# Kernel tuning notes

Measured on AMD Instinct MI355X. Metric: run time of the kernel, lower is better.

## Reference

```python
import jax, jax.numpy as jnp
import numpy as np

B, T, D, H, L = 512, 1024, 2, 32, 16  # batch, seq_len, input_dim, hidden_dim, latent_dim


def lstm_layer(x, W_ih, W_hh, b_ih, b_hh):
    """Single torch-semantics LSTM layer. x: [B, T, D_in] -> (h_seq [B,T,H], c_final [B,H]).
    Gate order matches torch: i, f, g, o."""
    Bb = x.shape[0]
    Hh = W_hh.shape[1]
    # Precompute input projection for all timesteps (one big GEMM).
    xW = jnp.einsum('btd,gd->btg', x, W_ih) + (b_ih + b_hh)  # [B, T, 4H]

    def step(carry, xw_t):
        h, c = carry
        gates = xw_t + h @ W_hh.T  # [B, 4H]
        i, f, g, o = jnp.split(gates, 4, axis=-1)
        i = jax.nn.sigmoid(i)
        f = jax.nn.sigmoid(f)
        g = jnp.tanh(g)
        o = jax.nn.sigmoid(o)
        c = f * c + i * g
        h = o * jnp.tanh(c)
        return (h, c), h

    h0 = jnp.zeros((Bb, Hh), x.dtype)
    c0 = jnp.zeros((Bb, Hh), x.dtype)
    (_, cT), h_seq = jax.lax.scan(step, (h0, c0), jnp.swapaxes(xW, 0, 1))
    return jnp.swapaxes(h_seq, 0, 1), cT


def setup_inputs() -> dict:
    key = jax.random.key(0)
    ks = jax.random.split(key, 20)
    s = 1.0 / np.sqrt(H)  # torch LSTM/Linear init scale
    u = lambda k, shape: jax.random.uniform(k, shape, jnp.float32, -s, s)
    inp = {"x": jax.random.normal(ks[0], (B, T, D), jnp.float32)}
    dims_in = [D, H, H]
    for l in range(3):
        inp[f"W_ih{l}"] = u(ks[1 + 4 * l], (4 * H, dims_in[l]))
        inp[f"W_hh{l}"] = u(ks[2 + 4 * l], (4 * H, H))
        inp[f"b_ih{l}"] = u(ks[3 + 4 * l], (4 * H,))
        inp[f"b_hh{l}"] = u(ks[4 + 4 * l], (4 * H,))
    inp["W_mean"] = u(ks[13], (L, H))
    inp["b_mean"] = u(ks[14], (L,))
    inp["W_logvar"] = u(ks[15], (L, H))
    inp["b_logvar"] = u(ks[16], (L,))
    return inp


def reference(x, W_ih0, W_hh0, b_ih0, b_hh0, W_ih1, W_hh1, b_ih1, b_hh1,
              W_ih2, W_hh2, b_ih2, b_hh2, W_mean, b_mean, W_logvar, b_logvar):
    # 3-layer LSTM (dropout inactive at inference); only top-layer final cell is used.
    h, _ = lstm_layer(x, W_ih0, W_hh0, b_ih0, b_hh0)
    h, _ = lstm_layer(h, W_ih1, W_hh1, b_ih1, b_hh1)
    _, c3 = lstm_layer(h, W_ih2, W_hh2, b_ih2, b_hh2)  # c3: [B, H]
    mean = c3 @ W_mean.T + b_mean        # [B, L]
    log_var = c3 @ W_logvar.T + b_logvar  # [B, L]
    return (mean, log_var)
```

## Files before the change

kernel.cpp:

```cpp
#include <hip/hip_runtime.h>

#define T_LEN 1024
#define HID   32
#define LDIM  16
#define BATCH 512
#define NT    384

typedef _Float16 h2 __attribute__((ext_vector_type(2)));
typedef unsigned int u32;

#if defined(__has_builtin)
#if __has_builtin(__builtin_amdgcn_fdot2)
#define HAVE_FDOT2 1
#endif
#if __has_builtin(__builtin_amdgcn_rcpf)
#define FAST_RCP(x) __builtin_amdgcn_rcpf(x)
#endif
#endif
#ifndef FAST_RCP
#define FAST_RCP(x) (1.0f / (x))
#endif

__device__ __forceinline__ float dot2acc(u32 w, u32 h, float acc) {
#ifdef HAVE_FDOT2
    return __builtin_amdgcn_fdot2(__builtin_bit_cast(h2, w),
                                  __builtin_bit_cast(h2, h), acc, false);
#else
    h2 a = __builtin_bit_cast(h2, w);
    h2 b = __builtin_bit_cast(h2, h);
    return acc + (float)a[0] * (float)b[0] + (float)a[1] * (float)b[1];
#endif
}

__device__ __forceinline__ u32 packh2(float a, float b) {
    h2 v;
    v[0] = (_Float16)a;
    v[1] = (_Float16)b;
    return __builtin_bit_cast(u32, v);
}

template <int OFF>
__device__ __forceinline__ float swz(float v) {
    return __builtin_bit_cast(float,
        __builtin_amdgcn_ds_swizzle(__builtin_bit_cast(int, v), OFF));
}

__global__ __launch_bounds__(NT, 3)
void lstm_encoder_kernel(const float* __restrict__ x,
                         const float* __restrict__ Wih0, const float* __restrict__ Whh0,
                         const float* __restrict__ bih0, const float* __restrict__ bhh0,
                         const float* __restrict__ Wih1, const float* __restrict__ Whh1,
                         const float* __restrict__ bih1, const float* __restrict__ bhh1,
                         const float* __restrict__ Wih2, const float* __restrict__ Whh2,
                         const float* __restrict__ bih2, const float* __restrict__ bhh2,
                         const float* __restrict__ Wm,  const float* __restrict__ bm,
                         const float* __restrict__ Wlv, const float* __restrict__ blv,
                         float* __restrict__ out)
{
    const int b    = blockIdx.x;
    const int tid  = threadIdx.x;
    const int lane = tid & 63;
    const int wave = tid >> 6;
    const int l    = wave >> 1;
    const int wv   = wave & 1;
    const int q    = (lane >> 3) & 3;
    const int e    = (lane & 7) | ((lane >> 2) & 8);
    const int j    = wv * 16 + e;
    const int r = ((q & 1) ? 64 : 0) + ((q & 2) ? 32 : 0) + j;

    __shared__ float xs[T_LEN * 2];
    __shared__ __align__(16) _Float16 hb0[3][HID];
    __shared__ __align__(16) _Float16 hb1[3][HID];
    __shared__ float cbuf[HID];

    const float4* xb4 = (const float4*)(x + (size_t)b * (T_LEN * 2));
    for (int i = tid; i < (T_LEN * 2) / 4; i += NT) ((float4*)xs)[i] = xb4[i];

    if (tid < 48)       ((u32*)hb0)[tid]      = 0u;
    else if (tid < 96)  ((u32*)hb1)[tid - 48] = 0u;

    const float* Wih = (l == 0) ? Wih0 : (l == 1) ? Wih1 : Wih2;
    const float* Whh = (l == 0) ? Whh0 : (l == 1) ? Whh1 : Whh2;
    const float* bih = (l == 0) ? bih0 : (l == 1) ? bih1 : bih2;
    const float* bhh = (l == 0) ? bhh0 : (l == 1) ? bhh1 : bhh2;

    u32 wpack[32];
    float wx0 = 0.f, wx1 = 0.f;
#pragma unroll
    for (int k = 0; k < 16; ++k)
        wpack[16 + k] = packh2(Whh[r * HID + 2 * k], Whh[r * HID + 2 * k + 1]);
    if (l == 0) {
        wx0 = Wih[r * 2 + 0];
        wx1 = Wih[r * 2 + 1];
#pragma unroll
        for (int k = 0; k < 16; ++k) wpack[k] = 0u;
    } else {
#pragma unroll
        for (int k = 0; k < 16; ++k)
            wpack[k] = packh2(Wih[r * HID + 2 * k], Wih[r * HID + 2 * k + 1]);
    }
    const float bias = bih[r] + bhh[r];
#pragma unroll
    for (int k = 0; k < 32; ++k) asm volatile("" : "+v"(wpack[k]));

    const bool  is_g = (q == 1);
    const float kneg = is_g ? -2.0f : -1.0f;
    const float mm   = is_g ?  2.0f :  1.0f;
    const float aa   = is_g ? -1.0f :  0.0f;

    float c = 0.0f;

    __syncthreads();

#define STEP(RD, WR, S)                                                          \
    do {                                                                         \
        const int t_ = (S) - l;                                                  \
        if ((unsigned)t_ < (unsigned)T_LEN) {                                    \
            float a0 = bias, a1 = 0.f, a2 = 0.f, a3 = 0.f;                       \
            if (l == 0) {                                                        \
                const float2 xv = *(const float2*)&xs[2 * t_];                   \
                a0 = fmaf(wx0, xv.x, a0);                                        \
                a1 = fmaf(wx1, xv.y, a1);                                        \
                const uint4* hv = (const uint4*)&RD[0][0];                       \
                _Pragma("unroll")                                                \
                for (int k = 0; k < 4; ++k) {                                    \
                    const uint4 h = hv[k];                                       \
                    a0 = dot2acc(wpack[16 + 4 * k + 0], h.x, a0);                \
                    a1 = dot2acc(wpack[16 + 4 * k + 1], h.y, a1);                \
                    a2 = dot2acc(wpack[16 + 4 * k + 2], h.z, a2);                \
                    a3 = dot2acc(wpack[16 + 4 * k + 3], h.w, a3);                \
                }                                                                \
            } else {                                                             \
                const uint4* hv = (const uint4*)&RD[l - 1][0];                   \
                _Pragma("unroll")                                                \
                for (int k = 0; k < 8; ++k) {                                    \
                    const uint4 h = hv[k];                                       \
                    a0 = dot2acc(wpack[4 * k + 0], h.x, a0);                     \
                    a1 = dot2acc(wpack[4 * k + 1], h.y, a1);                     \
                    a2 = dot2acc(wpack[4 * k + 2], h.z, a2);                     \
                    a3 = dot2acc(wpack[4 * k + 3], h.w, a3);                     \
                }                                                                \
            }                                                                    \
            const float pre = (a0 + a1) + (a2 + a3);                             \
            const float ex  = __expf(kneg * pre);                                \
            const float y   = fmaf(mm, FAST_RCP(1.0f + ex), aa);                 \
            const float y1  = swz<0x201F>(y);           \
            const float P   = y * y1;                   \
            const float v   = (q < 2) ? P : y;                                   \
            const float z   = swz<0x401F>(v);         \
            c = fmaf(y, c, z);                             \
            const float e2 = __expf(-2.0f * c);                                  \
            const float th = fmaf(2.0f, FAST_RCP(1.0f + e2), -1.0f);             \
            if (q == 2) WR[l][j] = (_Float16)(y1 * th);        \
        }                                                                        \
        __syncthreads();                                                         \
    } while (0)

    for (int s = 0; s < T_LEN + 2; s += 2) {
        STEP(hb0, hb1, s);
        STEP(hb1, hb0, s + 1);
    }
#undef STEP

    if (l == 2 && q == 2) cbuf[j] = c;
    __syncthreads();

    if (tid < 2 * LDIM) {
        const bool   is_mean = (tid < LDIM);
        const int    jo = is_mean ? tid : tid - LDIM;
        const float* W  = is_mean ? Wm  : Wlv;
        const float* Bb = is_mean ? bm  : blv;
        float acc = Bb[jo];
#pragma unroll
        for (int k = 0; k < HID; ++k) acc = fmaf(W[jo * HID + k], cbuf[k], acc);
        const size_t off = (is_mean ? 0 : (size_t)BATCH * LDIM) + (size_t)b * LDIM + jo;
        out[off] = acc;
    }
}

extern "C" void kernel_launch(void* const* d_in, const int* in_sizes, int n_in,
                              void* d_out, int out_size, void* d_ws, size_t ws_size,
                              hipStream_t stream) {
    const float* x    = (const float*)d_in[0];
    const float* Wih0 = (const float*)d_in[1];
    const float* Whh0 = (const float*)d_in[2];
    const float* bih0 = (const float*)d_in[3];
    const float* bhh0 = (const float*)d_in[4];
    const float* Wih1 = (const float*)d_in[5];
    const float* Whh1 = (const float*)d_in[6];
    const float* bih1 = (const float*)d_in[7];
    const float* bhh1 = (const float*)d_in[8];
    const float* Wih2 = (const float*)d_in[9];
    const float* Whh2 = (const float*)d_in[10];
    const float* bih2 = (const float*)d_in[11];
    const float* bhh2 = (const float*)d_in[12];
    const float* Wm   = (const float*)d_in[13];
    const float* bm   = (const float*)d_in[14];
    const float* Wlv  = (const float*)d_in[15];
    const float* blv  = (const float*)d_in[16];
    float* out = (float*)d_out;

    lstm_encoder_kernel<<<dim3(BATCH), dim3(NT), 0, stream>>>(
        x, Wih0, Whh0, bih0, bhh0, Wih1, Whh1, bih1, bhh1,
        Wih2, Whh2, bih2, bhh2, Wm, bm, Wlv, blv, out);
}
```

Baseline: 530.2 us.

## Batch 16 sequences per block and compute LSTM gates with MFMA

Each block now processes 16 batch elements instead of one. The per-step gate matmuls are replaced by 16x16x32 f16 MFMA instructions, with weights held in registers as A fragments and hidden states read from LDS as B fragments. The goal is to amortize the per-step barrier and dot-product cost across many sequences, and to use the matrix cores. In exchange the grid shrinks to 32 blocks, so most CUs on the chip sit idle. The gate math is reworked around exp2 with the weights pre-scaled by log2e, and the cell state is clamped to [-20, 20].

```diff
diff --git a/kernel.cpp b/kernel.cpp
--- a/kernel.cpp
+++ b/kernel.cpp
@@ -4,48 +4,37 @@
 #define HID   32
 #define LDIM  16
 #define BATCH 512
+#define NB    16
 #define NT    384
-
-typedef _Float16 h2 __attribute__((ext_vector_type(2)));
-typedef unsigned int u32;
+#define ROWB  80
+#define LAYB  (16 * ROWB)
+#define LOG2E 1.44269504f
+
+typedef _Float16 half8  __attribute__((ext_vector_type(8)));
+typedef _Float16 half2v __attribute__((ext_vector_type(2)));
+typedef float    f32x4  __attribute__((ext_vector_type(4)));
+typedef unsigned u32;
+typedef unsigned u32x4  __attribute__((ext_vector_type(4)));
+typedef unsigned u32x2  __attribute__((ext_vector_type(2)));
 
 #if defined(__has_builtin)
-#if __has_builtin(__builtin_amdgcn_fdot2)
-#define HAVE_FDOT2 1
-#endif
 #if __has_builtin(__builtin_amdgcn_rcpf)
 #define FAST_RCP(x) __builtin_amdgcn_rcpf(x)
 #endif
+#if __has_builtin(__builtin_amdgcn_exp2f)
+#define FAST_EXP2(x) __builtin_amdgcn_exp2f(x)
+#endif
 #endif
 #ifndef FAST_RCP
 #define FAST_RCP(x) (1.0f / (x))
 #endif
-
-__device__ __forceinline__ float dot2acc(u32 w, u32 h, float acc) {
-#ifdef HAVE_FDOT2
-    return __builtin_amdgcn_fdot2(__builtin_bit_cast(h2, w),
-                                  __builtin_bit_cast(h2, h), acc, false);
-#else
-    h2 a = __builtin_bit_cast(h2, w);
-    h2 b = __builtin_bit_cast(h2, h);
-    return acc + (float)a[0] * (float)b[0] + (float)a[1] * (float)b[1];
-#endif
-}
-
-__device__ __forceinline__ u32 packh2(float a, float b) {
-    h2 v;
-    v[0] = (_Float16)a;
-    v[1] = (_Float16)b;
-    return __builtin_bit_cast(u32, v);
-}
-
-template <int OFF>
-__device__ __forceinline__ float swz(float v) {
-    return __builtin_bit_cast(float,
-        __builtin_amdgcn_ds_swizzle(__builtin_bit_cast(int, v), OFF));
-}
-
-__global__ __launch_bounds__(NT, 3)
+#ifndef FAST_EXP2
+#define FAST_EXP2(x) __expf(0.69314718f * (x))
+#endif
+
+#define MFMA(a, b, c) __builtin_amdgcn_mfma_f32_16x16x32_f16((a), (b), (c), 0, 0, 0)
+
+__global__ __launch_bounds__(NT, 1)
 void lstm_encoder_kernel(const float* __restrict__ x,
                          const float* __restrict__ Wih0, const float* __restrict__ Whh0,
                          const float* __restrict__ bih0, const float* __restrict__ bhh0,
@@ -57,124 +46,139 @@
                          const float* __restrict__ Wlv, const float* __restrict__ blv,
                          float* __restrict__ out)
 {
-    const int b    = blockIdx.x;
+    const int b0   = blockIdx.x * NB;
     const int tid  = threadIdx.x;
     const int lane = tid & 63;
     const int wave = tid >> 6;
     const int l    = wave >> 1;
     const int wv   = wave & 1;
-    const int q    = (lane >> 3) & 3;
-    const int e    = (lane & 7) | ((lane >> 2) & 8);
-    const int j    = wv * 16 + e;
-    const int r = ((q & 1) ? 64 : 0) + ((q & 2) ? 32 : 0) + j;
-
-    __shared__ float xs[T_LEN * 2];
-    __shared__ __align__(16) _Float16 hb0[3][HID];
-    __shared__ __align__(16) _Float16 hb1[3][HID];
-    __shared__ float cbuf[HID];
-
-    const float4* xb4 = (const float4*)(x + (size_t)b * (T_LEN * 2));
-    for (int i = tid; i < (T_LEN * 2) / 4; i += NT) ((float4*)xs)[i] = xb4[i];
-
-    if (tid < 48)       ((u32*)hb0)[tid]      = 0u;
-    else if (tid < 96)  ((u32*)hb1)[tid - 48] = 0u;
+    const int n    = lane & 15;
+    const int kc   = lane >> 4;
+
+    __shared__ __align__(16) unsigned char hb_flat[2 * 3 * LAYB];
+    __shared__ float cbuf[NB * HID];
+
+    for (int i = tid; i < (int)(sizeof(hb_flat) / 4); i += NT) ((u32*)hb_flat)[i] = 0u;
 
     const float* Wih = (l == 0) ? Wih0 : (l == 1) ? Wih1 : Wih2;
     const float* Whh = (l == 0) ? Whh0 : (l == 1) ? Whh1 : Whh2;
     const float* bih = (l == 0) ? bih0 : (l == 1) ? bih1 : bih2;
     const float* bhh = (l == 0) ? bhh0 : (l == 1) ? bhh1 : bhh2;
 
-    u32 wpack[32];
-    float wx0 = 0.f, wx1 = 0.f;
-#pragma unroll
-    for (int k = 0; k < 16; ++k)
-        wpack[16 + k] = packh2(Whh[r * HID + 2 * k], Whh[r * HID + 2 * k + 1]);
-    if (l == 0) {
-        wx0 = Wih[r * 2 + 0];
-        wx1 = Wih[r * 2 + 1];
-#pragma unroll
-        for (int k = 0; k < 16; ++k) wpack[k] = 0u;
-    } else {
-#pragma unroll
-        for (int k = 0; k < 16; ++k)
-            wpack[k] = packh2(Wih[r * HID + 2 * k], Wih[r * HID + 2 * k + 1]);
-    }
-    const float bias = bih[r] + bhh[r];
-#pragma unroll
-    for (int k = 0; k < 32; ++k) asm volatile("" : "+v"(wpack[k]));
-
-    const bool  is_g = (q == 1);
-    const float kneg = is_g ? -2.0f : -1.0f;
-    const float mm   = is_g ?  2.0f :  1.0f;
-    const float aa   = is_g ? -1.0f :  0.0f;
-
-    float c = 0.0f;
+    half8 af[4][2];
+    f32x4 biasC[4];
+#pragma unroll
+    for (int tau = 0; tau < 4; ++tau) {
+        const int   R  = tau * HID + wv * 16 + n;
+        const float sc = (tau == 2) ? (2.0f * LOG2E) : LOG2E;
+#pragma unroll
+        for (int i2 = 0; i2 < 8; ++i2) {
+            const int kk = kc * 8 + i2;
+            const float w0 = (l == 0) ? Whh[R * HID + kk] : Wih[R * HID + kk];
+            const float w1 = (l == 0) ? ((kk < 2) ? Wih[R * 2 + kk] : 0.0f)
+                                      : Whh[R * HID + kk];
+            af[tau][0][i2] = (_Float16)(w0 * sc);
+            af[tau][1][i2] = (_Float16)(w1 * sc);
+        }
+#pragma unroll
+        for (int r = 0; r < 4; ++r) {
+            const int rr = tau * HID + wv * 16 + kc * 4 + r;
+            biasC[tau][r] = (bih[rr] + bhh[rr]) * sc;
+        }
+    }
+
+    const int off_r0 = ((l == 0) ? 0 : (l - 1)) * LAYB + n * ROWB + kc * 16;
+    const int off_r1 = l * LAYB + n * ROWB + kc * 16;
+    const int off_w  = l * LAYB + n * ROWB + (wv * 16 + kc * 4) * 2;
+
+    const float2* xb2 = (const float2*)(x + (size_t)(b0 + n) * (T_LEN * 2));
+    const bool xldr = (l == 0) && (kc == 0);
+    float2 xp0, xp1, xp2, xp3;
+    if (xldr) { xp0 = xb2[0]; xp1 = xb2[1]; xp2 = xb2[2]; xp3 = xb2[3]; }
+
+    float cc[4] = {0.f, 0.f, 0.f, 0.f};
 
     __syncthreads();
 
-#define STEP(RD, WR, S)                                                          \
+#define STEP(P, S, XP)                                                           \
     do {                                                                         \
         const int t_ = (S) - l;                                                  \
         if ((unsigned)t_ < (unsigned)T_LEN) {                                    \
-            float a0 = bias, a1 = 0.f, a2 = 0.f, a3 = 0.f;                       \
+            half8 bf0 = __builtin_bit_cast(half8,                                \
+                *(const u32x4*)(hb_flat + (P) * (3 * LAYB) + off_r0));           \
+            half8 bf1;                                                           \
             if (l == 0) {                                                        \
-                const float2 xv = *(const float2*)&xs[2 * t_];                   \
-                a0 = fmaf(wx0, xv.x, a0);                                        \
-                a1 = fmaf(wx1, xv.y, a1);                                        \
-                const uint4* hv = (const uint4*)&RD[0][0];                       \
-                _Pragma("unroll")                                                \
-                for (int k = 0; k < 4; ++k) {                                    \
-                    const uint4 h = hv[k];                                       \
-                    a0 = dot2acc(wpack[16 + 4 * k + 0], h.x, a0);                \
-                    a1 = dot2acc(wpack[16 + 4 * k + 1], h.y, a1);                \
-                    a2 = dot2acc(wpack[16 + 4 * k + 2], h.z, a2);                \
-                    a3 = dot2acc(wpack[16 + 4 * k + 3], h.w, a3);                \
-                }                                                                \
+                half8 z = {0, 0, 0, 0, 0, 0, 0, 0};                              \
+                if (kc == 0) { z[0] = (_Float16)XP.x; z[1] = (_Float16)XP.y; }   \
+                bf1 = z;                                                         \
             } else {                                                             \
-                const uint4* hv = (const uint4*)&RD[l - 1][0];                   \
-                _Pragma("unroll")                                                \
-                for (int k = 0; k < 8; ++k) {                                    \
-                    const uint4 h = hv[k];                                       \
-                    a0 = dot2acc(wpack[4 * k + 0], h.x, a0);                     \
-                    a1 = dot2acc(wpack[4 * k + 1], h.y, a1);                     \
-                    a2 = dot2acc(wpack[4 * k + 2], h.z, a2);                     \
-                    a3 = dot2acc(wpack[4 * k + 3], h.w, a3);                     \
-                }                                                                \
+                bf1 = __builtin_bit_cast(half8,                                  \
+                    *(const u32x4*)(hb_flat + (P) * (3 * LAYB) + off_r1));       \
             }                                                                    \
-            const float pre = (a0 + a1) + (a2 + a3);                             \
-            const float ex  = __expf(kneg * pre);                                \
-            const float y   = fmaf(mm, FAST_RCP(1.0f + ex), aa);                 \
-            const float y1  = swz<0x201F>(y);           \
-            const float P   = y * y1;                   \
-            const float v   = (q < 2) ? P : y;                                   \
-            const float z   = swz<0x401F>(v);         \
-            c = fmaf(y, c, z);                             \
-            const float e2 = __expf(-2.0f * c);                                  \
-            const float th = fmaf(2.0f, FAST_RCP(1.0f + e2), -1.0f);             \
-            if (q == 2) WR[l][j] = (_Float16)(y1 * th);        \
+            f32x4 ac0 = MFMA(af[0][0], bf0, biasC[0]);                           \
+            f32x4 ac1 = MFMA(af[1][0], bf0, biasC[1]);                           \
+            f32x4 ac2 = MFMA(af[2][0], bf0, biasC[2]);                           \
+            f32x4 ac3 = MFMA(af[3][0], bf0, biasC[3]);                           \
+            ac0 = MFMA(af[0][1], bf1, ac0);                                      \
+            ac1 = MFMA(af[1][1], bf1, ac1);                                      \
+            ac2 = MFMA(af[2][1], bf1, ac2);                                      \
+            ac3 = MFMA(af[3][1], bf1, ac3);                                      \
+            float hv[4];                                                         \
+            _Pragma("unroll")                                                    \
+            for (int r = 0; r < 4; ++r) {                                        \
+                const float ei = FAST_EXP2(-ac0[r]);    \
+                const float ef = FAST_EXP2(-ac1[r]);                             \
+                const float eg = FAST_EXP2(-ac2[r]);    \
+                const float eo = FAST_EXP2(-ac3[r]);                             \
+                const float ig = (1.0f - eg) *                                   \
+                                 FAST_RCP((1.0f + ei) * (1.0f + eg));            \
+                const float fv = FAST_RCP(1.0f + ef);                            \
+                float c_ = fmaf(fv, cc[r], ig);                                  \
+                c_ = fminf(fmaxf(c_, -20.0f), 20.0f);                            \
+                cc[r] = c_;                                                      \
+                const float ec = FAST_EXP2(-2.0f * LOG2E * c_);                  \
+                hv[r] = (1.0f - ec) *                                            \
+                        FAST_RCP((1.0f + eo) * (1.0f + ec));      \
+            }                                                                    \
+            half2v p01, p23;                                                     \
+            p01[0] = (_Float16)hv[0]; p01[1] = (_Float16)hv[1];                  \
+            p23[0] = (_Float16)hv[2]; p23[1] = (_Float16)hv[3];                  \
+            u32x2 wpk;                                                           \
+            wpk[0] = __builtin_bit_cast(u32, p01);                               \
+            wpk[1] = __builtin_bit_cast(u32, p23);                               \
+            *(u32x2*)(hb_flat + ((P) ^ 1) * (3 * LAYB) + off_w) = wpk;           \
         }                                                                        \
         __syncthreads();                                                         \
     } while (0)
 
     for (int s = 0; s < T_LEN + 2; s += 2) {
-        STEP(hb0, hb1, s);
-        STEP(hb1, hb0, s + 1);
+        STEP(0, s, xp0);
+        STEP(1, s + 1, xp1);
+        if (xldr) {
+            xp0 = xp2; xp1 = xp3;
+            const int t4 = (s + 4 < T_LEN) ? s + 4 : T_LEN - 1;
+            const int t5 = (s + 5 < T_LEN) ? s + 5 : T_LEN - 1;
+            xp2 = xb2[t4]; xp3 = xb2[t5];
+        }
     }
 #undef STEP
 
-    if (l == 2 && q == 2) cbuf[j] = c;
+    if (l == 2) {
+        float* cp = cbuf + n * HID + wv * 16 + kc * 4;
+        cp[0] = cc[0]; cp[1] = cc[1]; cp[2] = cc[2]; cp[3] = cc[3];
+    }
     __syncthreads();
 
-    if (tid < 2 * LDIM) {
-        const bool   is_mean = (tid < LDIM);
-        const int    jo = is_mean ? tid : tid - LDIM;
-        const float* W  = is_mean ? Wm  : Wlv;
-        const float* Bb = is_mean ? bm  : blv;
-        float acc = Bb[jo];
-#pragma unroll
-        for (int k = 0; k < HID; ++k) acc = fmaf(W[jo * HID + k], cbuf[k], acc);
-        const size_t off = (is_mean ? 0 : (size_t)BATCH * LDIM) + (size_t)b * LDIM + jo;
-        out[off] = acc;
+    for (int v = tid; v < NB * 2 * LDIM; v += NT) {
+        const int  nn = v >> 5;
+        const int  o  = v & 31;
+        const bool is_mean = (o < LDIM);
+        const int  jo = o & (LDIM - 1);
+        const float* W  = is_mean ? Wm : Wlv;
+        float acc = is_mean ? bm[jo] : blv[jo];
+#pragma unroll
+        for (int k = 0; k < HID; ++k) acc = fmaf(W[jo * HID + k], cbuf[nn * HID + k], acc);
+        out[(is_mean ? 0 : (size_t)BATCH * LDIM) + (size_t)(b0 + nn) * LDIM + jo] = acc;
     }
 }
 
@@ -200,7 +204,7 @@
     const float* blv  = (const float*)d_in[16];
     float* out = (float*)d_out;
 
-    lstm_encoder_kernel<<<dim3(BATCH), dim3(NT), 0, stream>>>(
+    lstm_encoder_kernel<<<dim3(BATCH / NB), dim3(NT), 0, stream>>>(
         x, Wih0, Whh0, bih0, bhh0, Wih1, Whh1, bih1, bhh1,
         Wih2, Whh2, bih2, bhh2, Wm, bm, Wlv, blv, out);
 }
```

After: 625.0 us. +17.9%, slower.
